# Performance work log

Hardware: AMD Instinct MI355X
Metric: run time of the kernel (lower is better)

The kernel has to match this reference:

```python
import jax, jax.numpy as jnp
import numpy as np

N_NODES = 50000
N_EDGES = 800000
IN_FEAT = 128
H_FEAT = 64
NUM_HEADS = 4
NEG_SLOPE = 0.2  # DGL GATConv default LeakyReLU slope


def _gat_conv(feat, src, dst, W, attn_l, attn_r, bias, num_heads, out_feats):
    # feat: [N, Din]; W: [Din, H*F]; attn_l/attn_r: [H, F]; bias: [H*F]
    N = feat.shape[0]
    h = (feat @ W).reshape(N, num_heads, out_feats)          # [N, H, F]
    el = jnp.sum(h * attn_l, axis=-1)                        # [N, H]
    er = jnp.sum(h * attn_r, axis=-1)                        # [N, H]
    e = jax.nn.leaky_relu(el[src] + er[dst], NEG_SLOPE)      # [E, H]
    # segment softmax over incoming edges of each destination node
    m = jax.ops.segment_max(e, dst, num_segments=N)          # [N, H]
    ex = jnp.exp(e - m[dst])                                 # [E, H]
    s = jax.ops.segment_sum(ex, dst, num_segments=N)         # [N, H]
    alpha = ex / s[dst]                                      # [E, H]
    # attn_drop omitted (eval-mode deterministic reference)
    msg = h[src] * alpha[:, :, None]                         # [E, H, F]
    out = jax.ops.segment_sum(msg, dst, num_segments=N)      # [N, H, F]
    return out + bias.reshape(1, num_heads, out_feats)


def setup_inputs() -> dict:
    key = jax.random.key(0)
    ks = jax.random.split(key, 16)
    feat = jax.random.normal(ks[0], (N_NODES, IN_FEAT), dtype=jnp.float32)
    src = jax.random.randint(ks[1], (N_EDGES,), 0, N_NODES)
    dst = jax.random.randint(ks[2], (N_EDGES,), 0, N_NODES)
    sc = 0.1
    H, F = NUM_HEADS, H_FEAT
    params = {
        'W1': jax.random.normal(ks[3], (IN_FEAT, H * F), dtype=jnp.float32) * sc,
        'al1': jax.random.normal(ks[4], (H, F), dtype=jnp.float32) * sc,
        'ar1': jax.random.normal(ks[5], (H, F), dtype=jnp.float32) * sc,
        'b1': jnp.zeros((H * F,), dtype=jnp.float32),
        'W2': jax.random.normal(ks[6], (H * F, H * F), dtype=jnp.float32) * sc,
        'al2': jax.random.normal(ks[7], (H, F), dtype=jnp.float32) * sc,
        'ar2': jax.random.normal(ks[8], (H, F), dtype=jnp.float32) * sc,
        'b2': jnp.zeros((H * F,), dtype=jnp.float32),
        'W3': jax.random.normal(ks[9], (H * F, F), dtype=jnp.float32) * sc,
        'al3': jax.random.normal(ks[10], (1, F), dtype=jnp.float32) * sc,
        'ar3': jax.random.normal(ks[11], (1, F), dtype=jnp.float32) * sc,
        'b3': jnp.zeros((F,), dtype=jnp.float32),
    }
    return {'feat': feat, 'src': src, 'dst': dst, **params}


def reference(feat, src, dst, W1, al1, ar1, b1, W2, al2, ar2, b2, W3, al3, ar3, b3):
    h = _gat_conv(feat, src, dst, W1, al1, ar1, b1, NUM_HEADS, H_FEAT)
    h = jax.nn.relu(h.reshape(h.shape[0], -1))               # flatten(1) + relu
    h = _gat_conv(h, src, dst, W2, al2, ar2, b2, NUM_HEADS, H_FEAT)
    h = jax.nn.relu(h.reshape(h.shape[0], -1))
    h = _gat_conv(h, src, dst, W3, al3, ar3, b3, 1, H_FEAT)
    return h.mean(axis=1)                                    # [N, h_feat]
```

## Files before the change

kernel.cpp:

```cpp
#include <hip/hip_runtime.h>
#include <math.h>

#define N_NODES 50000
#define N_EDGES 800000

typedef short bf8 __attribute__((ext_vector_type(8)));
typedef float f4x __attribute__((ext_vector_type(4)));
typedef float f2v __attribute__((ext_vector_type(2)));
typedef unsigned short us8 __attribute__((ext_vector_type(8)));

__device__ __forceinline__ unsigned short f2bf(float x) {
  unsigned u = __float_as_uint(x);
  unsigned r = (u + 0x7fff + ((u >> 16) & 1)) >> 16;
  return (unsigned short)r;
}
__device__ __forceinline__ float bf2f(unsigned short b) {
  return __uint_as_float(((unsigned)b) << 16);
}
__device__ __forceinline__ unsigned pack2(float lo, float hi) {
  return (unsigned)f2bf(lo) | ((unsigned)f2bf(hi) << 16);
}
__device__ __forceinline__ f2v bfpair(unsigned d) {
  f2v r;
  r.x = __uint_as_float(d << 16);
  r.y = __uint_as_float(d & 0xffff0000u);
  return r;
}

template <int ABF16>
__global__ __launch_bounds__(256) void gemm_mfma_k(
    const void* __restrict__ Xv, const float* __restrict__ W,
    unsigned short* __restrict__ Yb, float* __restrict__ el,
    float* __restrict__ er, const float* __restrict__ al,
    const float* __restrict__ ar, int N, int K, int M) {
  __shared__ unsigned short As[128][40];
  __shared__ unsigned short Bs[64][40];
  const int tile_n = blockIdx.x * 128;
  const int cb = blockIdx.y * 64;
  const int t = threadIdx.x;
  const int wave = t >> 6, lane = t & 63;
  const int quad = lane >> 4, l16 = lane & 15;

  f4x acc[2][4];
#pragma unroll
  for (int i = 0; i < 2; ++i)
#pragma unroll
    for (int j = 0; j < 4; ++j) acc[i][j] = (f4x){0.f, 0.f, 0.f, 0.f};

  const int ar_ = t >> 1;
  const int ac0 = (t & 1) * 16;
  const int bn = t & 63;
  const int bkq = t >> 6;

  for (int k0 = 0; k0 < K; k0 += 32) {
    if (ABF16) {
      const unsigned short* Xb = (const unsigned short*)Xv;
      int gr = tile_n + ar_;
      us8 u0 = (us8)0, u1 = (us8)0;
      if (gr < N) {
        const unsigned short* s = Xb + (size_t)gr * K + k0 + ac0;
        u0 = *(const us8*)(s + 0);
        u1 = *(const us8*)(s + 8);
      }
      *(us8*)&As[ar_][ac0] = u0;
      *(us8*)&As[ar_][ac0 + 8] = u1;
    } else {
      const float* X = (const float*)Xv;
      int gr = tile_n + ar_;
      uint4 u0, u1;
      if (gr < N) {
        const float* s = X + (size_t)gr * K + k0 + ac0;
        float4 a = *(const float4*)(s + 0);
        float4 b = *(const float4*)(s + 4);
        float4 c = *(const float4*)(s + 8);
        float4 d = *(const float4*)(s + 12);
        u0 = make_uint4(pack2(a.x, a.y), pack2(a.z, a.w),
                        pack2(b.x, b.y), pack2(b.z, b.w));
        u1 = make_uint4(pack2(c.x, c.y), pack2(c.z, c.w),
                        pack2(d.x, d.y), pack2(d.z, d.w));
      } else {
        u0 = make_uint4(0, 0, 0, 0);
        u1 = make_uint4(0, 0, 0, 0);
      }
      *(uint4*)&As[ar_][ac0] = u0;
      *(uint4*)&As[ar_][ac0 + 8] = u1;
    }
    {
      const float* s = W + (size_t)(k0 + bkq * 8) * M + cb + bn;
      float w0 = s[0 * M], w1 = s[1 * M], w2 = s[2 * M], w3 = s[3 * M];
      float w4 = s[4 * M], w5 = s[5 * M], w6 = s[6 * M], w7 = s[7 * M];
      uint4 u = make_uint4(pack2(w0, w1), pack2(w2, w3), pack2(w4, w5),
                           pack2(w6, w7));
      *(uint4*)&Bs[bn][bkq * 8] = u;
    }
    __syncthreads();
    bf8 afrag[2], bfrag[4];
#pragma unroll
    for (int rt = 0; rt < 2; ++rt)
      afrag[rt] = *(const bf8*)&As[wave * 32 + rt * 16 + l16][quad * 8];
#pragma unroll
    for (int ct = 0; ct < 4; ++ct)
      bfrag[ct] = *(const bf8*)&Bs[ct * 16 + l16][quad * 8];
#pragma unroll
    for (int rt = 0; rt < 2; ++rt)
#pragma unroll
      for (int ct = 0; ct < 4; ++ct)
        acc[rt][ct] = __builtin_amdgcn_mfma_f32_16x16x32_bf16(
            afrag[rt], bfrag[ct], acc[rt][ct], 0, 0, 0);
    __syncthreads();
  }
  const int H = M >> 6;
  const int head = cb >> 6;
  float al4[4], ar4[4];
#pragma unroll
  for (int ct = 0; ct < 4; ++ct) {
    al4[ct] = al[cb + ct * 16 + l16];
    ar4[ct] = ar[cb + ct * 16 + l16];
  }
#pragma unroll
  for (int rt = 0; rt < 2; ++rt) {
#pragma unroll
    for (int r = 0; r < 4; ++r) {
      int row = tile_n + wave * 32 + rt * 16 + quad * 4 + r;
      float pl = 0.f, pr = 0.f;
#pragma unroll
      for (int ct = 0; ct < 4; ++ct) {
        float y = acc[rt][ct][r];
        pl += y * al4[ct];
        pr += y * ar4[ct];
        if (row < N) Yb[(size_t)row * M + cb + ct * 16 + l16] = f2bf(y);
      }
#pragma unroll
      for (int off = 1; off < 16; off <<= 1) {
        pl += __shfl_xor(pl, off);
        pr += __shfl_xor(pr, off);
      }
      if (l16 == 0 && row < N) {
        el[row * H + head] = pl;
        er[row * H + head] = pr;
      }
    }
  }
}

__global__ __launch_bounds__(256) void count_deg_k(
    const int4* __restrict__ dst4, int* __restrict__ deg, int E4) {
  int i = blockIdx.x * blockDim.x + threadIdx.x;
  if (i < E4) {
    int4 d = dst4[i];
    atomicAdd(&deg[d.x], 1);
    atomicAdd(&deg[d.y], 1);
    atomicAdd(&deg[d.z], 1);
    atomicAdd(&deg[d.w], 1);
  }
}

__global__ __launch_bounds__(256) void alloc_rows_k(
    const int* __restrict__ deg, int* __restrict__ rowstart,
    int* __restrict__ cursor, int* __restrict__ gcounter, int N) {
  int i = blockIdx.x * blockDim.x + threadIdx.x;
  int lane = threadIdx.x & 63;
  int d = (i < N) ? deg[i] : 0;
  int x = d;
#pragma unroll
  for (int off = 1; off < 64; off <<= 1) {
    int t = __shfl_up(x, off);
    if (lane >= off) x += t;
  }
  int wsum = __shfl(x, 63);
  int base = 0;
  if (lane == 63) base = atomicAdd(gcounter, wsum);
  base = __shfl(base, 63);
  if (i < N) {
    int mystart = base + x - d;
    rowstart[i] = mystart;
    cursor[i] = mystart;
  }
}

__global__ __launch_bounds__(256) void scatter_k(
    const int4* __restrict__ src4, const int4* __restrict__ dst4,
    int* __restrict__ cursor, int* __restrict__ src_sorted, int E4) {
  int i = blockIdx.x * blockDim.x + threadIdx.x;
  if (i < E4) {
    int4 s = src4[i];
    int4 d = dst4[i];
    int p0 = atomicAdd(&cursor[d.x], 1);
    src_sorted[p0] = s.x;
    int p1 = atomicAdd(&cursor[d.y], 1);
    src_sorted[p1] = s.y;
    int p2 = atomicAdd(&cursor[d.z], 1);
    src_sorted[p2] = s.z;
    int p3 = atomicAdd(&cursor[d.w], 1);
    src_sorted[p3] = s.w;
  }
}

template <int RELU>
__global__ __launch_bounds__(256) void node_agg4_k(
    const unsigned short* __restrict__ hb, const float* __restrict__ el,
    const float* __restrict__ er, const int* __restrict__ rowstart,
    const int* __restrict__ rowend, const int* __restrict__ src_sorted,
    const float* __restrict__ bias, unsigned short* __restrict__ outb,
    int N) {
  int node = blockIdx.x * 4 + (threadIdx.x >> 6);
  int lane = threadIdx.x & 63;
  if (node >= N) return;
  int start = rowstart[node], end = rowend[node];
  int e16 = lane & 15;
  int headA = lane >> 4;
  int eslot = lane >> 5;
  int flane = lane & 31;
  int fo8 = flane << 3;
  int headf = fo8 >> 6;
  float er_a = er[node * 4 + headA];
  f2v acc2[4];
#pragma unroll
  for (int q = 0; q < 4; ++q) acc2[q] = (f2v){0.f, 0.f};
  float ssum = 0.f;
  for (int c0 = start; c0 < end; c0 += 16) {
    int p = c0 + e16;
    bool v = p < end;
    int s = v ? src_sorted[p] : 0;
    float e = el[s * 4 + headA] + er_a;
    e = (e >= 0.f) ? e : 0.2f * e;
    float ex = v ? __expf(e) : 0.f;
    ssum += ex;
    int sjv[8];
    float ajv[8];
#pragma unroll
    for (int jj = 0; jj < 8; ++jj) {
      int idx = (2 * jj + eslot) | (headf << 4);
      sjv[jj] = __shfl(s, idx);
      ajv[jj] = __shfl(ex, idx);
    }
    int nch = end - c0;
    if (nch > 16) nch = 16;
    int nj = (nch + 1) >> 1;
#pragma unroll 8
    for (int jj = 0; jj < nj; ++jj) {
      uint4 d = *(const uint4*)(hb + (size_t)sjv[jj] * 256 + fo8);
      f2v a2 = (f2v){ajv[jj], ajv[jj]};
      acc2[0] += bfpair(d.x) * a2;
      acc2[1] += bfpair(d.y) * a2;
      acc2[2] += bfpair(d.z) * a2;
      acc2[3] += bfpair(d.w) * a2;
    }
  }
#pragma unroll
  for (int off = 1; off < 16; off <<= 1) ssum += __shfl_xor(ssum, off);
  float sden = __shfl(ssum, headf << 4);
  float acc[8];
#pragma unroll
  for (int q = 0; q < 4; ++q) {
    acc[2 * q] = acc2[q].x;
    acc[2 * q + 1] = acc2[q].y;
  }
#pragma unroll
  for (int q = 0; q < 8; ++q) acc[q] += __shfl_xor(acc[q], 32);
  float inv = (end > start) ? 1.f / sden : 0.f;
  if (eslot == 0) {
    us8 o;
#pragma unroll
    for (int q = 0; q < 8; ++q) {
      float vv = acc[q] * inv + bias[fo8 + q];
      if (RELU) vv = fmaxf(vv, 0.f);
      o[q] = f2bf(vv);
    }
    *(us8*)(outb + (size_t)node * 256 + fo8) = o;
  }
}

__global__ __launch_bounds__(256) void node_agg1_k(
    const unsigned short* __restrict__ hb, const float* __restrict__ el,
    const float* __restrict__ er, const int* __restrict__ rowstart,
    const int* __restrict__ rowend, const int* __restrict__ src_sorted,
    const float* __restrict__ bias, float* __restrict__ out, int N) {
  int node = blockIdx.x * 4 + (threadIdx.x >> 6);
  int lane = threadIdx.x & 63;
  if (node >= N) return;
  int start = rowstart[node], end = rowend[node];
  int eslot = lane >> 3;
  int fo8 = (lane & 7) << 3;
  float er_v = er[node];
  f2v acc2[4];
#pragma unroll
  for (int q = 0; q < 4; ++q) acc2[q] = (f2v){0.f, 0.f};
  float ssum = 0.f;
  for (int c0 = start; c0 < end; c0 += 64) {
    int p = c0 + lane;
    bool v = p < end;
    int s = v ? src_sorted[p] : 0;
    float e = el[s] + er_v;
    e = (e >= 0.f) ? e : 0.2f * e;
    float ex = v ? __expf(e) : 0.f;
    ssum += ex;
    int nch = end - c0;
    if (nch > 64) nch = 64;
    int nj = (nch + 7) >> 3;
#pragma unroll 8
    for (int jj = 0; jj < nj; ++jj) {
      int idx = jj * 8 + eslot;
      int sj = __shfl(s, idx);
      float aj = __shfl(ex, idx);
      uint4 d = *(const uint4*)(hb + (size_t)sj * 64 + fo8);
      f2v a2 = (f2v){aj, aj};
      acc2[0] += bfpair(d.x) * a2;
      acc2[1] += bfpair(d.y) * a2;
      acc2[2] += bfpair(d.z) * a2;
      acc2[3] += bfpair(d.w) * a2;
    }
  }
#pragma unroll
  for (int off = 1; off < 64; off <<= 1) ssum += __shfl_xor(ssum, off);
  float acc[8];
#pragma unroll
  for (int q = 0; q < 4; ++q) {
    acc[2 * q] = acc2[q].x;
    acc[2 * q + 1] = acc2[q].y;
  }
#pragma unroll
  for (int off = 8; off < 64; off <<= 1)
#pragma unroll
    for (int q = 0; q < 8; ++q) acc[q] += __shfl_xor(acc[q], off);
  float inv = (end > start) ? 1.f / ssum : 0.f;
  if (eslot == 0) {
    float* o = out + (size_t)node * 64 + fo8;
#pragma unroll
    for (int q = 0; q < 8; ++q) o[q] = acc[q] * inv + bias[fo8 + q];
  }
}

extern "C" void kernel_launch(void* const* d_in, const int* in_sizes, int n_in,
                              void* d_out, int out_size, void* d_ws,
                              size_t ws_size, hipStream_t stream) {
  const float* feat = (const float*)d_in[0];
  const int* src = (const int*)d_in[1];
  const int* dst = (const int*)d_in[2];
  const float* W1 = (const float*)d_in[3];
  const float* al1 = (const float*)d_in[4];
  const float* ar1 = (const float*)d_in[5];
  const float* b1 = (const float*)d_in[6];
  const float* W2 = (const float*)d_in[7];
  const float* al2 = (const float*)d_in[8];
  const float* ar2 = (const float*)d_in[9];
  const float* b2 = (const float*)d_in[10];
  const float* W3 = (const float*)d_in[11];
  const float* al3 = (const float*)d_in[12];
  const float* ar3 = (const float*)d_in[13];
  const float* b3 = (const float*)d_in[14];
  float* out = (float*)d_out;

  unsigned short* hb = (unsigned short*)d_ws;
  unsigned short* fb = hb + (size_t)N_NODES * 256;
  float* el = (float*)(fb + (size_t)N_NODES * 256);
  float* er = el + (size_t)N_NODES * 4;
  int* rowstart = (int*)(er + (size_t)N_NODES * 4);
  int* cursor = rowstart + N_NODES;
  int* deg = cursor + N_NODES;
  int* gcounter = deg + N_NODES;
  int* src_sorted = gcounter + 1;

  const int N = N_NODES, E = N_EDGES;
  const int E4 = E / 4;
  const int GX = (N + 127) / 128;

  hipMemsetAsync(deg, 0, (size_t)(N + 1) * sizeof(int), stream);
  hipLaunchKernelGGL(count_deg_k, dim3((E4 + 255) / 256), dim3(256), 0, stream,
                     (const int4*)dst, deg, E4);
  hipLaunchKernelGGL(alloc_rows_k, dim3((N + 255) / 256), dim3(256), 0, stream,
                     deg, rowstart, cursor, gcounter, N);
  hipLaunchKernelGGL(scatter_k, dim3((E4 + 255) / 256), dim3(256), 0, stream,
                     (const int4*)src, (const int4*)dst, cursor, src_sorted,
                     E4);

  hipLaunchKernelGGL((gemm_mfma_k<0>), dim3(GX, 4), dim3(256), 0, stream, feat,
                     W1, hb, el, er, al1, ar1, N, 128, 256);
  hipLaunchKernelGGL((node_agg4_k<1>), dim3((N + 3) / 4), dim3(256), 0, stream,
                     hb, el, er, rowstart, cursor, src_sorted, b1, fb, N);

  hipLaunchKernelGGL((gemm_mfma_k<1>), dim3(GX, 4), dim3(256), 0, stream, fb,
                     W2, hb, el, er, al2, ar2, N, 256, 256);
  hipLaunchKernelGGL((node_agg4_k<1>), dim3((N + 3) / 4), dim3(256), 0, stream,
                     hb, el, er, rowstart, cursor, src_sorted, b2, fb, N);

  hipLaunchKernelGGL((gemm_mfma_k<1>), dim3(GX, 1), dim3(256), 0, stream, fb,
                     W3, hb, el, er, al3, ar3, N, 256, 64);
  hipLaunchKernelGGL(node_agg1_k, dim3((N + 3) / 4), dim3(256), 0, stream, hb,
                     el, er, rowstart, cursor, src_sorted, b3, out, N);
}
```

Baseline: 415.9 us.

## Make aggregation kernels persistent with software-prefetched edge chunks and next-node rows

The three node aggregation kernels become grid-stride persistent kernels launched with 2048 blocks. Each wave walks several nodes, keeps the bias in registers, and prefetches the next chunk's source indices and el values, including the first chunk of the next node, while the current chunk's gathers run. The aim is to hide the dependent index-then-el load latency and cut block launch overhead. In exchange it uses more registers, adds loop-carried state, and risks load imbalance from a fixed grid size.

After: 421.0 us. Within noise of the previous version (+1.2%).

```diff
diff --git a/kernel.cpp b/kernel.cpp
--- a/kernel.cpp
+++ b/kernel.cpp
@@ -203,71 +203,107 @@
     const int* __restrict__ rowend, const int* __restrict__ src_sorted,
     const float* __restrict__ bias, unsigned short* __restrict__ outb,
     int N) {
-  int node = blockIdx.x * 4 + (threadIdx.x >> 6);
-  int lane = threadIdx.x & 63;
+  const int lane = threadIdx.x & 63;
+  const int e16 = lane & 15;
+  const int headA = lane >> 4;
+  const int eslot = lane >> 5;
+  const int flane = lane & 31;
+  const int fo8 = flane << 3;
+  const int headf = fo8 >> 6;
+  const int wid = blockIdx.x * 4 + (threadIdx.x >> 6);
+  const int wstep = gridDim.x << 2;
+  float bq[8];
+#pragma unroll
+  for (int q = 0; q < 8; ++q) bq[q] = bias[fo8 + q];
+
+  int node = wid;
   if (node >= N) return;
   int start = rowstart[node], end = rowend[node];
-  int e16 = lane & 15;
-  int headA = lane >> 4;
-  int eslot = lane >> 5;
-  int flane = lane & 31;
-  int fo8 = flane << 3;
-  int headf = fo8 >> 6;
   float er_a = er[node * 4 + headA];
-  f2v acc2[4];
-#pragma unroll
-  for (int q = 0; q < 4; ++q) acc2[q] = (f2v){0.f, 0.f};
-  float ssum = 0.f;
-  for (int c0 = start; c0 < end; c0 += 16) {
-    int p = c0 + e16;
-    bool v = p < end;
-    int s = v ? src_sorted[p] : 0;
-    float e = el[s * 4 + headA] + er_a;
-    e = (e >= 0.f) ? e : 0.2f * e;
-    float ex = v ? __expf(e) : 0.f;
-    ssum += ex;
-    int sjv[8];
-    float ajv[8];
-#pragma unroll
-    for (int jj = 0; jj < 8; ++jj) {
-      int idx = (2 * jj + eslot) | (headf << 4);
-      sjv[jj] = __shfl(s, idx);
-      ajv[jj] = __shfl(ex, idx);
-    }
-    int nch = end - c0;
-    if (nch > 16) nch = 16;
-    int nj = (nch + 1) >> 1;
+  int p = start + e16;
+  bool v = p < end;
+  int s = v ? src_sorted[p] : 0;
+  float elv = el[s * 4 + headA];
+
+  while (true) {
+    int nnode = node + wstep;
+    int nstart = 0, nend = 0;
+    float ner = 0.f;
+    if (nnode < N) {
+      nstart = rowstart[nnode];
+      nend = rowend[nnode];
+      ner = er[nnode * 4 + headA];
+    }
+    f2v acc2[4];
+#pragma unroll
+    for (int q = 0; q < 4; ++q) acc2[q] = (f2v){0.f, 0.f};
+    float ssum = 0.f;
+    int c0 = start;
+    do {
+      float e = elv + er_a;
+      e = (e >= 0.f) ? e : 0.2f * e;
+      float ex = v ? __expf(e) : 0.f;
+      ssum += ex;
+      bool lastc = (c0 + 16 >= end);
+      int pb = lastc ? nstart : (c0 + 16);
+      int plim = lastc ? nend : end;
+      int p2 = pb + e16;
+      bool v2 = p2 < plim;
+      int s2 = v2 ? src_sorted[p2] : 0;
+      float elv2 = el[s2 * 4 + headA];
+      int sjv[8];
+      float ajv[8];
+#pragma unroll
+      for (int jj = 0; jj < 8; ++jj) {
+        int idx = (2 * jj + eslot) | (headf << 4);
+        sjv[jj] = __shfl(s, idx);
+        ajv[jj] = __shfl(ex, idx);
+      }
+      int nch = end - c0;
+      if (nch > 16) nch = 16;
+      int nj = (nch + 1) >> 1;
 #pragma unroll 8
-    for (int jj = 0; jj < nj; ++jj) {
-      uint4 d = *(const uint4*)(hb + (size_t)sjv[jj] * 256 + fo8);
-      f2v a2 = (f2v){ajv[jj], ajv[jj]};
-      acc2[0] += bfpair(d.x) * a2;
-      acc2[1] += bfpair(d.y) * a2;
-      acc2[2] += bfpair(d.z) * a2;
-      acc2[3] += bfpair(d.w) * a2;
-    }
-  }
-#pragma unroll
-  for (int off = 1; off < 16; off <<= 1) ssum += __shfl_xor(ssum, off);
-  float sden = __shfl(ssum, headf << 4);
-  float acc[8];
-#pragma unroll
-  for (int q = 0; q < 4; ++q) {
-    acc[2 * q] = acc2[q].x;
-    acc[2 * q + 1] = acc2[q].y;
-  }
-#pragma unroll
-  for (int q = 0; q < 8; ++q) acc[q] += __shfl_xor(acc[q], 32);
-  float inv = (end > start) ? 1.f / sden : 0.f;
-  if (eslot == 0) {
-    us8 o;
-#pragma unroll
-    for (int q = 0; q < 8; ++q) {
-      float vv = acc[q] * inv + bias[fo8 + q];
-      if (RELU) vv = fmaxf(vv, 0.f);
-      o[q] = f2bf(vv);
-    }
-    *(us8*)(outb + (size_t)node * 256 + fo8) = o;
+      for (int jj = 0; jj < nj; ++jj) {
+        uint4 d = *(const uint4*)(hb + (size_t)sjv[jj] * 256 + fo8);
+        f2v a2 = (f2v){ajv[jj], ajv[jj]};
+        acc2[0] += bfpair(d.x) * a2;
+        acc2[1] += bfpair(d.y) * a2;
+        acc2[2] += bfpair(d.z) * a2;
+        acc2[3] += bfpair(d.w) * a2;
+      }
+      s = s2;
+      v = v2;
+      elv = elv2;
+      c0 += 16;
+    } while (c0 < end);
+    float ssr = ssum;
+#pragma unroll
+    for (int off = 1; off < 16; off <<= 1) ssr += __shfl_xor(ssr, off);
+    float sden = __shfl(ssr, headf << 4);
+    float acc[8];
+#pragma unroll
+    for (int q = 0; q < 4; ++q) {
+      acc[2 * q] = acc2[q].x;
+      acc[2 * q + 1] = acc2[q].y;
+    }
+#pragma unroll
+    for (int q = 0; q < 8; ++q) acc[q] += __shfl_xor(acc[q], 32);
+    float inv = (end > start) ? 1.f / sden : 0.f;
+    if (eslot == 0) {
+      us8 o;
+#pragma unroll
+      for (int q = 0; q < 8; ++q) {
+        float vv = acc[q] * inv + bq[q];
+        if (RELU) vv = fmaxf(vv, 0.f);
+        o[q] = f2bf(vv);
+      }
+      *(us8*)(outb + (size_t)node * 256 + fo8) = o;
+    }
+    node = nnode;
+    if (node >= N) break;
+    start = nstart;
+    end = nend;
+    er_a = ner;
   }
 }
 
@@ -276,58 +312,94 @@
     const float* __restrict__ er, const int* __restrict__ rowstart,
     const int* __restrict__ rowend, const int* __restrict__ src_sorted,
     const float* __restrict__ bias, float* __restrict__ out, int N) {
-  int node = blockIdx.x * 4 + (threadIdx.x >> 6);
-  int lane = threadIdx.x & 63;
+  const int lane = threadIdx.x & 63;
+  const int eslot = lane >> 3;
+  const int fo8 = (lane & 7) << 3;
+  const int wid = blockIdx.x * 4 + (threadIdx.x >> 6);
+  const int wstep = gridDim.x << 2;
+  float bq[8];
+#pragma unroll
+  for (int q = 0; q < 8; ++q) bq[q] = bias[fo8 + q];
+
+  int node = wid;
   if (node >= N) return;
   int start = rowstart[node], end = rowend[node];
-  int eslot = lane >> 3;
-  int fo8 = (lane & 7) << 3;
   float er_v = er[node];
-  f2v acc2[4];
-#pragma unroll
-  for (int q = 0; q < 4; ++q) acc2[q] = (f2v){0.f, 0.f};
-  float ssum = 0.f;
-  for (int c0 = start; c0 < end; c0 += 64) {
-    int p = c0 + lane;
-    bool v = p < end;
-    int s = v ? src_sorted[p] : 0;
-    float e = el[s] + er_v;
-    e = (e >= 0.f) ? e : 0.2f * e;
-    float ex = v ? __expf(e) : 0.f;
-    ssum += ex;
-    int nch = end - c0;
-    if (nch > 64) nch = 64;
-    int nj = (nch + 7) >> 3;
+  int p = start + lane;
+  bool v = p < end;
+  int s = v ? src_sorted[p] : 0;
+  float elv = el[s];
+
+  while (true) {
+    int nnode = node + wstep;
+    int nstart = 0, nend = 0;
+    float ner = 0.f;
+    if (nnode < N) {
+      nstart = rowstart[nnode];
+      nend = rowend[nnode];
+      ner = er[nnode];
+    }
+    f2v acc2[4];
+#pragma unroll
+    for (int q = 0; q < 4; ++q) acc2[q] = (f2v){0.f, 0.f};
+    float ssum = 0.f;
+    int c0 = start;
+    do {
+      float e = elv + er_v;
+      e = (e >= 0.f) ? e : 0.2f * e;
+      float ex = v ? __expf(e) : 0.f;
+      ssum += ex;
+      bool lastc = (c0 + 64 >= end);
+      int pb = lastc ? nstart : (c0 + 64);
+      int plim = lastc ? nend : end;
+      int p2 = pb + lane;
+      bool v2 = p2 < plim;
+      int s2 = v2 ? src_sorted[p2] : 0;
+      float elv2 = el[s2];
+      int nch = end - c0;
+      if (nch > 64) nch = 64;
+      int nj = (nch + 7) >> 3;
 #pragma unroll 8
-    for (int jj = 0; jj < nj; ++jj) {
-      int idx = jj * 8 + eslot;
-      int sj = __shfl(s, idx);
-      float aj = __shfl(ex, idx);
-      uint4 d = *(const uint4*)(hb + (size_t)sj * 64 + fo8);
-      f2v a2 = (f2v){aj, aj};
-      acc2[0] += bfpair(d.x) * a2;
-      acc2[1] += bfpair(d.y) * a2;
-      acc2[2] += bfpair(d.z) * a2;
-      acc2[3] += bfpair(d.w) * a2;
-    }
-  }
-#pragma unroll
-  for (int off = 1; off < 64; off <<= 1) ssum += __shfl_xor(ssum, off);
-  float acc[8];
-#pragma unroll
-  for (int q = 0; q < 4; ++q) {
-    acc[2 * q] = acc2[q].x;
-    acc[2 * q + 1] = acc2[q].y;
-  }
-#pragma unroll
-  for (int off = 8; off < 64; off <<= 1)
-#pragma unroll
-    for (int q = 0; q < 8; ++q) acc[q] += __shfl_xor(acc[q], off);
-  float inv = (end > start) ? 1.f / ssum : 0.f;
-  if (eslot == 0) {
-    float* o = out + (size_t)node * 64 + fo8;
-#pragma unroll
-    for (int q = 0; q < 8; ++q) o[q] = acc[q] * inv + bias[fo8 + q];
+      for (int jj = 0; jj < nj; ++jj) {
+        int idx = jj * 8 + eslot;
+        int sj = __shfl(s, idx);
+        float aj = __shfl(ex, idx);
+        uint4 d = *(const uint4*)(hb + (size_t)sj * 64 + fo8);
+        f2v a2 = (f2v){aj, aj};
+        acc2[0] += bfpair(d.x) * a2;
+        acc2[1] += bfpair(d.y) * a2;
+        acc2[2] += bfpair(d.z) * a2;
+        acc2[3] += bfpair(d.w) * a2;
+      }
+      s = s2;
+      v = v2;
+      elv = elv2;
+      c0 += 64;
+    } while (c0 < end);
+    float ssr = ssum;
+#pragma unroll
+    for (int off = 1; off < 64; off <<= 1) ssr += __shfl_xor(ssr, off);
+    float acc[8];
+#pragma unroll
+    for (int q = 0; q < 4; ++q) {
+      acc[2 * q] = acc2[q].x;
+      acc[2 * q + 1] = acc2[q].y;
+    }
+#pragma unroll
+    for (int off = 8; off < 64; off <<= 1)
+#pragma unroll
+      for (int q = 0; q < 8; ++q) acc[q] += __shfl_xor(acc[q], off);
+    float inv = (end > start) ? 1.f / ssr : 0.f;
+    if (eslot == 0) {
+      float* o = out + (size_t)node * 64 + fo8;
+#pragma unroll
+      for (int q = 0; q < 8; ++q) o[q] = acc[q] * inv + bq[q];
+    }
+    node = nnode;
+    if (node >= N) break;
+    start = nstart;
+    end = nend;
+    er_v = ner;
   }
 }
 
@@ -376,16 +448,16 @@
 
   hipLaunchKernelGGL((gemm_mfma_k<0>), dim3(GX, 4), dim3(256), 0, stream, feat,
                      W1, hb, el, er, al1, ar1, N, 128, 256);
-  hipLaunchKernelGGL((node_agg4_k<1>), dim3((N + 3) / 4), dim3(256), 0, stream,
-                     hb, el, er, rowstart, cursor, src_sorted, b1, fb, N);
+  hipLaunchKernelGGL((node_agg4_k<1>), dim3(2048), dim3(256), 0, stream, hb,
+                     el, er, rowstart, cursor, src_sorted, b1, fb, N);
 
   hipLaunchKernelGGL((gemm_mfma_k<1>), dim3(GX, 4), dim3(256), 0, stream, fb,
                      W2, hb, el, er, al2, ar2, N, 256, 256);
-  hipLaunchKernelGGL((node_agg4_k<1>), dim3((N + 3) / 4), dim3(256), 0, stream,
-                     hb, el, er, rowstart, cursor, src_sorted, b2, fb, N);
+  hipLaunchKernelGGL((node_agg4_k<1>), dim3(2048), dim3(256), 0, stream, hb,
+                     el, er, rowstart, cursor, src_sorted, b2, fb, N);
 
   hipLaunchKernelGGL((gemm_mfma_k<1>), dim3(GX, 1), dim3(256), 0, stream, fb,
                      W3, hb, el, er, al3, ar3, N, 256, 64);
-  hipLaunchKernelGGL(node_agg1_k, dim3((N + 3) / 4), dim3(256), 0, stream, hb,
-                     el, er, rowstart, cursor, src_sorted, b3, out, N);
-}
+  hipLaunchKernelGGL(node_agg1_k, dim3(2048), dim3(256), 0, stream, hb, el, er,
+                     rowstart, cursor, src_sorted, b3, out, N);
+}
```
